# Performance work log

Hardware: AMD Instinct MI355X
Metric: run time of the kernel (lower is better)

The kernel has to match this reference:

```python
import jax, jax.numpy as jnp
import numpy as np

B, N, D = 8192, 1024, 3


def setup_inputs() -> dict:
    key = jax.random.key(0)
    k1, k2, k3, k4 = jax.random.split(key, 4)
    return {
        "x": jax.random.normal(k1, (B, N, D), dtype=jnp.float32),
        "mu_x": jax.random.normal(k2, (B, D), dtype=jnp.float32),
        "y": jax.random.normal(k3, (B, N, D), dtype=jnp.float32),
        "mu_y": jax.random.normal(k4, (B, D), dtype=jnp.float32),
    }


def reference(x, mu_x, y, mu_y):
    # Center both point clouds: [B, N, 3]
    xc = x - mu_x[:, None, :]
    yc = y - mu_y[:, None, :]
    # Cross-covariance per batch: [B, 3, 3]
    cov = jnp.einsum('bnd,bne->bde', xc, yc)
    # Batched 3x3 SVD; square matrices so full_matrices=False matches torch
    U, S, Vt = jnp.linalg.svd(cov, full_matrices=False)
    R = jnp.matmul(U, Vt)  # [B, 3, 3] (no det sign correction, as in source)
    # Frobenius norm over (points, dims) per batch
    xn = jnp.sqrt(jnp.sum(xc * xc, axis=(1, 2)))
    yn = jnp.sqrt(jnp.sum(yc * yc, axis=(1, 2)))
    scale_factor_S = yn / (xn + 1e-6)  # [B]
    # Translation: t = mu_y - R @ mu_x
    t = mu_y - jnp.einsum('bij,bj->bi', R, mu_x)  # [B, 3]
    return (R, t, scale_factor_S)
```

## Files before the change

kernel.cpp:

```cpp
#include <hip/hip_runtime.h>

#define NB 8192
#define NPTS 1024


__global__ __launch_bounds__(256) void cov_kernel(
    const float* __restrict__ x, const float* __restrict__ y,
    const float* __restrict__ mu_x, const float* __restrict__ mu_y,
    float* __restrict__ ws)
{
    const int wave = threadIdx.x >> 6;
    const int lane = threadIdx.x & 63;
    const int b    = blockIdx.x * 4 + wave;

    const float4* x4 = (const float4*)(x + (size_t)b * (NPTS * 3));
    const float4* y4 = (const float4*)(y + (size_t)b * (NPTS * 3));

    const float mx0 = mu_x[b * 3 + 0], mx1 = mu_x[b * 3 + 1], mx2 = mu_x[b * 3 + 2];
    const float my0 = mu_y[b * 3 + 0], my1 = mu_y[b * 3 + 1], my2 = mu_y[b * 3 + 2];

    float v[11];
    #pragma unroll
    for (int i = 0; i < 11; ++i) v[i] = 0.0f;

    #pragma unroll
    for (int c = 0; c < 4; ++c) {
        const int base = 3 * (c * 64 + lane);
        const float4 xa = x4[base + 0], xb4 = x4[base + 1], xc4 = x4[base + 2];
        const float4 ya = y4[base + 0], yb4 = y4[base + 1], yc4 = y4[base + 2];

        const float xp[4][3] = {{xa.x, xa.y, xa.z}, {xa.w, xb4.x, xb4.y},
                                {xb4.z, xb4.w, xc4.x}, {xc4.y, xc4.z, xc4.w}};
        const float yp[4][3] = {{ya.x, ya.y, ya.z}, {ya.w, yb4.x, yb4.y},
                                {yb4.z, yb4.w, yc4.x}, {yc4.y, yc4.z, yc4.w}};

        #pragma unroll
        for (int k = 0; k < 4; ++k) {
            const float xd0 = xp[k][0] - mx0, xd1 = xp[k][1] - mx1, xd2 = xp[k][2] - mx2;
            const float yd0 = yp[k][0] - my0, yd1 = yp[k][1] - my1, yd2 = yp[k][2] - my2;
            v[0] += xd0 * yd0; v[1] += xd0 * yd1; v[2] += xd0 * yd2;
            v[3] += xd1 * yd0; v[4] += xd1 * yd1; v[5] += xd1 * yd2;
            v[6] += xd2 * yd0; v[7] += xd2 * yd1; v[8] += xd2 * yd2;
            v[9]  += xd0 * xd0 + xd1 * xd1 + xd2 * xd2;
            v[10] += yd0 * yd0 + yd1 * yd1 + yd2 * yd2;
        }
    }

    #pragma unroll
    for (int off = 32; off >= 1; off >>= 1) {
        #pragma unroll
        for (int i = 0; i < 11; ++i) v[i] += __shfl_xor(v[i], off, 64);
    }

    if (lane == 0) {
        float* w = ws + (size_t)b * 12;
        #pragma unroll
        for (int i = 0; i < 11; ++i) w[i] = v[i];
    }
}

__global__ __launch_bounds__(256) void polar_kernel(
    const float* __restrict__ ws,
    const float* __restrict__ mu_x, const float* __restrict__ mu_y,
    float* __restrict__ out)
{
    const int b = blockIdx.x * 256 + threadIdx.x;

    const float4* w4 = (const float4*)ws + 3 * (size_t)b;
    const float4 w0 = w4[0], w1 = w4[1], w2 = w4[2];

    float Q[9] = {w0.x, w0.y, w0.z, w0.w, w1.x, w1.y, w1.z, w1.w, w2.x};
    const float nxx = w2.y;
    const float nyy = w2.z;

    #pragma unroll
    for (int it = 0; it < 11; ++it) {
        float C[9];
        C[0] = Q[4] * Q[8] - Q[5] * Q[7];
        C[1] = Q[5] * Q[6] - Q[3] * Q[8];
        C[2] = Q[3] * Q[7] - Q[4] * Q[6];
        C[3] = Q[2] * Q[7] - Q[1] * Q[8];
        C[4] = Q[0] * Q[8] - Q[2] * Q[6];
        C[5] = Q[1] * Q[6] - Q[0] * Q[7];
        C[6] = Q[1] * Q[5] - Q[2] * Q[4];
        C[7] = Q[2] * Q[3] - Q[0] * Q[5];
        C[8] = Q[0] * Q[4] - Q[1] * Q[3];
        const float det = Q[0] * C[0] + Q[1] * C[1] + Q[2] * C[2];
        const float invdet = 1.0f / det;

        float nq = 0.0f, nc = 0.0f;
        #pragma unroll
        for (int i = 0; i < 9; ++i) { nq += Q[i] * Q[i]; nc += C[i] * C[i]; }
        const float g  = sqrtf(sqrtf(nc * invdet * invdet / nq));
        const float hg = 0.5f * g;
        const float hi = 0.5f * invdet / g;
        #pragma unroll
        for (int i = 0; i < 9; ++i) Q[i] = hg * Q[i] + hi * C[i];
    }

    const float mx0 = mu_x[b * 3 + 0], mx1 = mu_x[b * 3 + 1], mx2 = mu_x[b * 3 + 2];
    const float my0 = mu_y[b * 3 + 0], my1 = mu_y[b * 3 + 1], my2 = mu_y[b * 3 + 2];

    #pragma unroll
    for (int i = 0; i < 9; ++i) out[(size_t)b * 9 + i] = Q[i];

    float* tout = out + (size_t)NB * 9 + (size_t)b * 3;
    tout[0] = my0 - (Q[0] * mx0 + Q[1] * mx1 + Q[2] * mx2);
    tout[1] = my1 - (Q[3] * mx0 + Q[4] * mx1 + Q[5] * mx2);
    tout[2] = my2 - (Q[6] * mx0 + Q[7] * mx1 + Q[8] * mx2);

    out[(size_t)NB * 12 + b] = sqrtf(nyy) / (sqrtf(nxx) + 1e-6f);
}

extern "C" void kernel_launch(void* const* d_in, const int* in_sizes, int n_in,
                              void* d_out, int out_size, void* d_ws, size_t ws_size,
                              hipStream_t stream) {
    const float* x    = (const float*)d_in[0];
    const float* mu_x = (const float*)d_in[1];
    const float* y    = (const float*)d_in[2];
    const float* mu_y = (const float*)d_in[3];
    float* out = (float*)d_out;
    float* ws  = (float*)d_ws;

    cov_kernel<<<dim3(NB / 4), dim3(256), 0, stream>>>(x, y, mu_x, mu_y, ws);
    polar_kernel<<<dim3(NB / 256), dim3(256), 0, stream>>>(ws, mu_x, mu_y, out);
}
```

Measured before the change: 219.9 us.

## Stage point clouds through LDS with one block per batch; use fast rcp/sqrt

The covariance kernel now assigns one 256-thread block per batch instead of one wave per batch. It loads x and y with fully coalesced float4 reads into shared memory, then has each thread pull its four contiguous points back out of LDS. Partial sums are reduced across the four waves through a small shared array. The polar iteration replaces IEEE division and sqrt with the hardware rcp/sqrt intrinsics, trading some accuracy for fewer instructions. This adds LDS traffic and two barriers per block.

```diff
diff --git a/kernel.cpp b/kernel.cpp
--- a/kernel.cpp
+++ b/kernel.cpp
@@ -9,41 +9,47 @@
     const float* __restrict__ mu_x, const float* __restrict__ mu_y,
     float* __restrict__ ws)
 {
-    const int wave = threadIdx.x >> 6;
-    const int lane = threadIdx.x & 63;
-    const int b    = blockIdx.x * 4 + wave;
+    __shared__ float4 sx[768];
+    __shared__ float4 sy[768];
+    __shared__ float red[4][12];
+
+    const int t = threadIdx.x;
+    const int b = blockIdx.x;
 
     const float4* x4 = (const float4*)(x + (size_t)b * (NPTS * 3));
     const float4* y4 = (const float4*)(y + (size_t)b * (NPTS * 3));
 
+    const float4 a0 = x4[t], a1 = x4[t + 256], a2 = x4[t + 512];
+    const float4 c0 = y4[t], c1 = y4[t + 256], c2 = y4[t + 512];
+
     const float mx0 = mu_x[b * 3 + 0], mx1 = mu_x[b * 3 + 1], mx2 = mu_x[b * 3 + 2];
     const float my0 = mu_y[b * 3 + 0], my1 = mu_y[b * 3 + 1], my2 = mu_y[b * 3 + 2];
+
+    sx[t] = a0; sx[t + 256] = a1; sx[t + 512] = a2;
+    sy[t] = c0; sy[t + 256] = c1; sy[t + 512] = c2;
+    __syncthreads();
+
+    const float4 xa = sx[3 * t + 0], xb4 = sx[3 * t + 1], xc4 = sx[3 * t + 2];
+    const float4 ya = sy[3 * t + 0], yb4 = sy[3 * t + 1], yc4 = sy[3 * t + 2];
+
+    const float xp[4][3] = {{xa.x, xa.y, xa.z}, {xa.w, xb4.x, xb4.y},
+                            {xb4.z, xb4.w, xc4.x}, {xc4.y, xc4.z, xc4.w}};
+    const float yp[4][3] = {{ya.x, ya.y, ya.z}, {ya.w, yb4.x, yb4.y},
+                            {yb4.z, yb4.w, yc4.x}, {yc4.y, yc4.z, yc4.w}};
 
     float v[11];
     #pragma unroll
     for (int i = 0; i < 11; ++i) v[i] = 0.0f;
 
     #pragma unroll
-    for (int c = 0; c < 4; ++c) {
-        const int base = 3 * (c * 64 + lane);
-        const float4 xa = x4[base + 0], xb4 = x4[base + 1], xc4 = x4[base + 2];
-        const float4 ya = y4[base + 0], yb4 = y4[base + 1], yc4 = y4[base + 2];
-
-        const float xp[4][3] = {{xa.x, xa.y, xa.z}, {xa.w, xb4.x, xb4.y},
-                                {xb4.z, xb4.w, xc4.x}, {xc4.y, xc4.z, xc4.w}};
-        const float yp[4][3] = {{ya.x, ya.y, ya.z}, {ya.w, yb4.x, yb4.y},
-                                {yb4.z, yb4.w, yc4.x}, {yc4.y, yc4.z, yc4.w}};
-
-        #pragma unroll
-        for (int k = 0; k < 4; ++k) {
-            const float xd0 = xp[k][0] - mx0, xd1 = xp[k][1] - mx1, xd2 = xp[k][2] - mx2;
-            const float yd0 = yp[k][0] - my0, yd1 = yp[k][1] - my1, yd2 = yp[k][2] - my2;
-            v[0] += xd0 * yd0; v[1] += xd0 * yd1; v[2] += xd0 * yd2;
-            v[3] += xd1 * yd0; v[4] += xd1 * yd1; v[5] += xd1 * yd2;
-            v[6] += xd2 * yd0; v[7] += xd2 * yd1; v[8] += xd2 * yd2;
-            v[9]  += xd0 * xd0 + xd1 * xd1 + xd2 * xd2;
-            v[10] += yd0 * yd0 + yd1 * yd1 + yd2 * yd2;
-        }
+    for (int k = 0; k < 4; ++k) {
+        const float xd0 = xp[k][0] - mx0, xd1 = xp[k][1] - mx1, xd2 = xp[k][2] - mx2;
+        const float yd0 = yp[k][0] - my0, yd1 = yp[k][1] - my1, yd2 = yp[k][2] - my2;
+        v[0] += xd0 * yd0; v[1] += xd0 * yd1; v[2] += xd0 * yd2;
+        v[3] += xd1 * yd0; v[4] += xd1 * yd1; v[5] += xd1 * yd2;
+        v[6] += xd2 * yd0; v[7] += xd2 * yd1; v[8] += xd2 * yd2;
+        v[9]  += xd0 * xd0 + xd1 * xd1 + xd2 * xd2;
+        v[10] += yd0 * yd0 + yd1 * yd1 + yd2 * yd2;
     }
 
     #pragma unroll
@@ -52,10 +58,14 @@
         for (int i = 0; i < 11; ++i) v[i] += __shfl_xor(v[i], off, 64);
     }
 
-    if (lane == 0) {
-        float* w = ws + (size_t)b * 12;
+    if ((t & 63) == 0) {
         #pragma unroll
-        for (int i = 0; i < 11; ++i) w[i] = v[i];
+        for (int i = 0; i < 11; ++i) red[t >> 6][i] = v[i];
+    }
+    __syncthreads();
+
+    if (t < 11) {
+        ws[(size_t)b * 12 + t] = red[0][t] + red[1][t] + red[2][t] + red[3][t];
     }
 }
 
@@ -86,14 +96,15 @@
         C[7] = Q[2] * Q[3] - Q[0] * Q[5];
         C[8] = Q[0] * Q[4] - Q[1] * Q[3];
         const float det = Q[0] * C[0] + Q[1] * C[1] + Q[2] * C[2];
-        const float invdet = 1.0f / det;
+        const float invdet = __builtin_amdgcn_rcpf(det);
 
         float nq = 0.0f, nc = 0.0f;
         #pragma unroll
         for (int i = 0; i < 9; ++i) { nq += Q[i] * Q[i]; nc += C[i] * C[i]; }
-        const float g  = sqrtf(sqrtf(nc * invdet * invdet / nq));
+        const float g  = __builtin_amdgcn_sqrtf(__builtin_amdgcn_sqrtf(
+                             nc * invdet * invdet * __builtin_amdgcn_rcpf(nq)));
         const float hg = 0.5f * g;
-        const float hi = 0.5f * invdet / g;
+        const float hi = 0.5f * invdet * __builtin_amdgcn_rcpf(g);
         #pragma unroll
         for (int i = 0; i < 9; ++i) Q[i] = hg * Q[i] + hi * C[i];
     }
@@ -122,6 +133,6 @@
     float* out = (float*)d_out;
     float* ws  = (float*)d_ws;
 
-    cov_kernel<<<dim3(NB / 4), dim3(256), 0, stream>>>(x, y, mu_x, mu_y, ws);
+    cov_kernel<<<dim3(NB), dim3(256), 0, stream>>>(x, y, mu_x, mu_y, ws);
     polar_kernel<<<dim3(NB / 256), dim3(256), 0, stream>>>(ws, mu_x, mu_y, out);
 }
```

After: 217.3 us. No clear change (-1.2%).
